# Kernel tuning notes

Hardware: AMD Instinct MI355X
Metric: run time of the kernel (lower is better)

## Reference

```python
import jax, jax.numpy as jnp
import numpy as np

L = 24        # n_layer
E = 1024      # n_emb
H = 4 * E     # ffn hidden
V = 50277     # vocab
LN_EPS = 1e-5


def _ln(x, w, b):
    m = x.mean(-1, keepdims=True)
    v = ((x - m) ** 2).mean(-1, keepdims=True)
    return (x - m) / jnp.sqrt(v + LN_EPS) * w + b


def setup_inputs() -> dict:
    key = jax.random.key(0)
    ks = jax.random.split(key, 24)
    s = 1.0 / np.sqrt(E)      # keep matvec outputs O(1) so exp-recurrence is stable
    sh = 1.0 / np.sqrt(H)
    inp = {
        "emb":      jax.random.normal(ks[0], (V, E), jnp.float32) * 0.02,
        "ln0_w":    jnp.ones((E,), jnp.float32),
        "ln0_b":    jnp.zeros((E,), jnp.float32),
        "ln1_w":    jnp.ones((L, E), jnp.float32),
        "ln1_b":    jnp.zeros((L, E), jnp.float32),
        "att_tmk":  jax.random.uniform(ks[1], (L, E), jnp.float32),
        "att_tmv":  jax.random.uniform(ks[2], (L, E), jnp.float32),
        "att_tmr":  jax.random.uniform(ks[3], (L, E), jnp.float32),
        "att_tf":   jax.random.normal(ks[4], (L, E), jnp.float32) * 0.3,
        # checkpoint stores raw time_decay; loader applies -exp(.)
        "att_td":   -jnp.exp(jax.random.normal(ks[5], (L, E), jnp.float32) * 0.3),
        "att_kw":   jax.random.normal(ks[6], (L, E, E), jnp.float32) * s,
        "att_vw":   jax.random.normal(ks[7], (L, E, E), jnp.float32) * s,
        "att_rw":   jax.random.normal(ks[8], (L, E, E), jnp.float32) * s,
        "att_ow":   jax.random.normal(ks[9], (L, E, E), jnp.float32) * s,
        "ln2_w":    jnp.ones((L, E), jnp.float32),
        "ln2_b":    jnp.zeros((L, E), jnp.float32),
        "ffn_tmk":  jax.random.uniform(ks[10], (L, E), jnp.float32),
        "ffn_tmr":  jax.random.uniform(ks[11], (L, E), jnp.float32),
        "ffn_kw":   jax.random.normal(ks[12], (L, H, E), jnp.float32) * s,
        "ffn_vw":   jax.random.normal(ks[13], (L, E, H), jnp.float32) * sh,
        "ffn_rw":   jax.random.normal(ks[14], (L, E, E), jnp.float32) * s,
        "ln_out_w": jnp.ones((E,), jnp.float32),
        "ln_out_b": jnp.zeros((E,), jnp.float32),
        "head_w":   jax.random.normal(ks[15], (V, E), jnp.float32) * s,
        "token":    123,
    }
    state = jnp.zeros((5 * L, E), jnp.float32)
    state = state.at[4::5].set(-1e30)  # pp slot, as in empty_state()
    inp["state"] = state
    return inp


def _rwkv_forward(emb, ln0_w, ln0_b, ln1_w, ln1_b, att_tmk, att_tmv, att_tmr,
                  att_tf, att_td, att_kw, att_vw, att_rw, att_ow,
                  ln2_w, ln2_b, ffn_tmk, ffn_tmr, ffn_kw, ffn_vw, ffn_rw,
                  ln_out_w, ln_out_b, head_w, state, token):
    x = emb[token]
    x = _ln(x, ln0_w, ln0_b)           # blocks.0.ln0 applied once before layer 0
    st = state.reshape(L, 5, E)        # slots: (ffn_x, att_x, aa, bb, pp)

    def step(x, inp):
        (s, l1w, l1b, tmk, tmv, tmr, tf, td, kw, vw, rw, ow,
         l2w, l2b, ftmk, ftmr, fkw, fvw, frw) = inp
        ffn_x, att_x, aa, bb, pp = s[0], s[1], s[2], s[3], s[4]
        # --- time-mix (SA) ---
        xn = _ln(x, l1w, l1b)
        xk = xn * tmk + att_x * (1 - tmk)
        xv = xn * tmv + att_x * (1 - tmv)
        xr = xn * tmr + att_x * (1 - tmr)
        r = jax.nn.sigmoid(rw @ xr)
        k = kw @ xk
        v = vw @ xv
        # numerically-stabilized WKV output
        ww = tf + k
        p = jnp.maximum(pp, ww)
        e1 = jnp.exp(pp - p)
        e2 = jnp.exp(ww - p)
        a = e1 * aa + e2 * v
        b = e1 * bb + e2
        # state update
        ww2 = pp + td
        p2 = jnp.maximum(ww2, k)
        f1 = jnp.exp(ww2 - p2)
        f2 = jnp.exp(k - p2)
        naa = f1 * aa + f2 * v
        nbb = f1 * bb + f2
        npp = p2
        sx = x + ow @ (r * a / b)
        # --- channel-mix (FF) ---
        xn2 = _ln(sx, l2w, l2b)
        fxk = xn2 * ftmk + ffn_x * (1 - ftmk)
        fxr = xn2 * ftmr + ffn_x * (1 - ftmr)
        fr = jax.nn.sigmoid(frw @ fxr)
        fk = jnp.square(jax.nn.relu(fkw @ fxk))
        out = sx + fr * (fvw @ fk)
        new_s = jnp.stack([xn2, xn, naa, nbb, npp])
        return out, new_s

    xs = (st, ln1_w, ln1_b, att_tmk, att_tmv, att_tmr, att_tf, att_td,
          att_kw, att_vw, att_rw, att_ow, ln2_w, ln2_b, ffn_tmk, ffn_tmr,
          ffn_kw, ffn_vw, ffn_rw)
    x, new_st = jax.lax.scan(step, x, xs)
    logits = head_w @ _ln(x, ln_out_w, ln_out_b)
    return logits, new_st.reshape(5 * L, E)


def reference(emb, ln0_w, ln0_b, ln1_w, ln1_b, att_tmk, att_tmv, att_tmr,
              att_tf, att_td, att_kw, att_vw, att_rw, att_ow,
              ln2_w, ln2_b, ffn_tmk, ffn_tmr, ffn_kw, ffn_vw, ffn_rw,
              ln_out_w, ln_out_b, head_w, state, token):
    return _rwkv_forward(emb, ln0_w, ln0_b, ln1_w, ln1_b, att_tmk, att_tmv,
                         att_tmr, att_tf, att_td, att_kw, att_vw, att_rw,
                         att_ow, ln2_w, ln2_b, ffn_tmk, ffn_tmr, ffn_kw,
                         ffn_vw, ffn_rw, ln_out_w, ln_out_b, head_w,
                         state, token)
```

## Files before the change

### kernel.cpp

```cpp
#include <hip/hip_runtime.h>

#define E 1024
#define H 4096
#define NLAYER 24
#define V 50277
#define NB 256
#define NT 1024
#define LN_EPS 1e-5f

typedef unsigned long long u64;

#define R1O    0
#define R2O    16384
#define POOLO  32768
#define SXO    36864
#define SSXO   37888
#define FXRO   38912
#define REDO   39936
#define PARTO  39968
#define PART2O 39984
#define SMEMF  40000

struct Params {
  const float* emb;   const float* ln0_w; const float* ln0_b;
  const float* ln1_w; const float* ln1_b;
  const float* tmk;   const float* tmv;   const float* tmr;
  const float* tf;    const float* td;
  const float* kw;    const float* vw;    const float* rw;  const float* ow;
  const float* ln2_w; const float* ln2_b;
  const float* ftmk;  const float* ftmr;
  const float* fkw;   const float* fvw;   const float* frw;
  const float* lnow;  const float* lnob;  const float* headw;
  const float* st;    const int* tok;
  float* out; float* ws;
};

__device__ __forceinline__ void stg_tag(u64* p, float v, unsigned tag) {
  u64 w = ((u64)__float_as_uint(v) << 32) | (u64)tag;
  __hip_atomic_store(p, w, __ATOMIC_RELAXED, __HIP_MEMORY_SCOPE_AGENT);
}
__device__ __forceinline__ u64 ld_tag(const u64* p) {
  return __hip_atomic_load(p, __ATOMIC_RELAXED, __HIP_MEMORY_SCOPE_AGENT);
}
__device__ __forceinline__ float poll_tag(const u64* p, unsigned tag) {
  u64 w = ld_tag(p);
  while ((unsigned)w != tag) { __builtin_amdgcn_s_sleep(1); w = ld_tag(p); }
  return __uint_as_float((unsigned)(w >> 32));
}

__device__ __forceinline__ void wait_pf() {
  asm volatile("s_waitcnt vmcnt(0)" ::: "memory");
}

__device__ __forceinline__ void gload_lds16(const float* g, float* l) {
  __builtin_amdgcn_global_load_lds(
      (const __attribute__((address_space(1))) unsigned int*)(g),
      (__attribute__((address_space(3))) unsigned int*)(l), 16, 0, 0);
}
__device__ __forceinline__ void pf_row4k(const float* row, float* dst, int lane) {
#pragma unroll
  for (int c = 0; c < 4; ++c)
    gload_lds16(row + c * 256 + lane * 4, dst + c * 256);
}

__device__ __forceinline__ float warp_sum(float v) {
#pragma unroll
  for (int off = 32; off; off >>= 1) v += __shfl_down(v, off);
  return v;
}

__device__ __forceinline__ float2 ln_stats(float v, float* red) {
  float a = v, b = v * v;
#pragma unroll
  for (int off = 32; off; off >>= 1) { a += __shfl_xor(a, off); b += __shfl_xor(b, off); }
  const int wid = threadIdx.x >> 6, lane = threadIdx.x & 63;
  if (lane == 0) { red[2 * wid] = a; red[2 * wid + 1] = b; }
  __syncthreads();
  float s1 = 0.f, s2 = 0.f;
  const float2* r2 = (const float2*)red;
#pragma unroll
  for (int j = 0; j < 16; ++j) { float2 t = r2[j]; s1 += t.x; s2 += t.y; }
  float m = s1 * (1.f / E);
  return make_float2(m, s2 * (1.f / E) - m * m);
}

__device__ __forceinline__ float dot4(float4 a, float4 b) {
  return a.x * b.x + a.y * b.y + a.z * b.z + a.w * b.w;
}

__device__ __forceinline__ float dotlds(const float* wrow, const float* vec, int lane) {
  const float4* w4 = (const float4*)wrow;
  const float4* v4 = (const float4*)vec;
  float acc = 0.f;
#pragma unroll
  for (int p = 0; p < 4; ++p)
    acc += dot4(w4[lane + p * 64], v4[lane + p * 64]);
  return warp_sum(acc);
}

__global__ __launch_bounds__(NT, 1) void rwkv_kernel(Params p) {
  const int tid = threadIdx.x, bid = blockIdx.x;
  const int lane = tid & 63, wid = tid >> 6;

  extern __shared__ float smem[];
  float* r1     = smem + R1O;
  float* r2     = smem + R2O;
  float* pool   = smem + POOLO;
  float* s_x    = smem + SXO;
  float* s_sx   = smem + SSXO;
  float* s_fxr  = smem + FXRO;
  float* s_red  = smem + REDO;
  float* s_part = smem + PARTO;
  float* s_part2= smem + PART2O;

  u64* tws = (u64*)p.ws;
  u64* tk  = tws;
  u64* tv  = tws + 2 * E;
  u64* tr  = tws + 4 * E;
  u64* tsx = tws + 6 * E;
  u64* tx  = tws + 8 * E;
  u64* tfk = tws + 10 * E;

  float* out_st = p.out + V;
  const int token = p.tok[0];

  const bool hasA = wid < 12;
  const int rA = bid * 12 + wid;
  const int matA = rA >> 10, rmA = rA & (E - 1);
  const int rloc = wid >> 2, kc = wid & 3;
  const int rowO = bid * 4 + rloc;
  float* wA = r1 + wid * 1024;
  float* wD = r2 + rloc * 4096 + kc * 1024;

  if (hasA) {
    const float* W = (matA == 0 ? p.kw : matA == 1 ? p.vw : p.rw) + (size_t)rmA * E;
    pf_row4k(W, wA, lane);
  }

  {
    float v = p.emb[(size_t)token * E + tid];
    float2 mv = ln_stats(v, s_red);
    s_x[tid] = (v - mv.x) / sqrtf(mv.y + LN_EPS) * p.ln0_w[tid] + p.ln0_b[tid];
  }

  for (int l = 0; l < NLAYER; ++l) {
    const float* stl = p.st + (size_t)5 * l * E;
    float* ostl = out_st + (size_t)5 * l * E;
    const int par = l & 1;
    const unsigned tg = (unsigned)(l + 1);

    float l1w = p.ln1_w[l * E + tid], l1b = p.ln1_b[l * E + tid];
    float ax = stl[E + tid];
    float ta = p.tmk[l * E + tid], tb = p.tmv[l * E + tid], tc = p.tmr[l * E + tid];
    float xv_;
    if (l > 0) { xv_ = poll_tag(&tx[par * E + tid], (unsigned)l); s_x[tid] = xv_; }
    else       { xv_ = s_x[tid]; }
    {
      float2 mv = ln_stats(xv_, s_red);
      float xn = (xv_ - mv.x) / sqrtf(mv.y + LN_EPS) * l1w + l1b;
      pool[tid]        = xn * ta + ax * (1.f - ta);
      pool[1024 + tid] = xn * tb + ax * (1.f - tb);
      pool[2048 + tid] = xn * tc + ax * (1.f - tc);
      if (bid == 0) ostl[E + tid] = xn;
    }
    __syncthreads();
    wait_pf();
    if (hasA) {
      float d = dotlds(wA, pool + matA * 1024, lane);
      if (lane == 0) {
        u64* dst = (matA == 0 ? tk : matA == 1 ? tv : tr) + par * E + rmA;
        stg_tag(dst, matA == 2 ? 1.f / (1.f + expf(-d)) : d, tg);
      }
    }

    {
      float aav = stl[2 * E + tid], bbv = stl[3 * E + tid], ppv = stl[4 * E + tid];
      float tfv = p.tf[l * E + tid], tdv = p.td[l * E + tid];
      float4 wow = ((const float4*)(p.ow + (size_t)l * E * E + (size_t)rowO * E + kc * 256))[lane];
      pf_row4k(p.fkw + (size_t)l * H * E + (size_t)(bid * 16 + wid) * E, wA, lane);
      const u64 *bk = tk + par * E + tid, *bv = tv + par * E + tid, *br = tr + par * E + tid;
      u64 wk = ld_tag(bk), wv = ld_tag(bv), wr = ld_tag(br);
      while ((unsigned)wk != tg) { __builtin_amdgcn_s_sleep(1); wk = ld_tag(bk); }
      while ((unsigned)wv != tg) { __builtin_amdgcn_s_sleep(1); wv = ld_tag(bv); }
      while ((unsigned)wr != tg) { __builtin_amdgcn_s_sleep(1); wr = ld_tag(br); }
      float kk = __uint_as_float((unsigned)(wk >> 32));
      float vv = __uint_as_float((unsigned)(wv >> 32));
      float rr = __uint_as_float((unsigned)(wr >> 32));
      float wwv = tfv + kk;
      float pm = fmaxf(ppv, wwv);
      float e1 = expf(ppv - pm), e2 = expf(wwv - pm);
      float a = e1 * aav + e2 * vv, b = e1 * bbv + e2;
      pool[3072 + tid] = rr * a / b;
      float ww2 = ppv + tdv;
      float p2 = fmaxf(ww2, kk);
      float f1 = expf(ww2 - p2), f2 = expf(kk - p2);
      if (bid == 0) {
        ostl[2 * E + tid] = f1 * aav + f2 * vv;
        ostl[3 * E + tid] = f1 * bbv + f2;
        ostl[4 * E + tid] = p2;
      }
      __syncthreads();
      const float4* v4 = (const float4*)(pool + 3072 + kc * 256);
      float acc = warp_sum(dot4(wow, v4[lane]));
      if (lane == 0) s_part[wid] = acc;
    }
    __syncthreads();
    if (tid < 4) {
      float dsum = s_part[tid * 4] + s_part[tid * 4 + 1] +
                   s_part[tid * 4 + 2] + s_part[tid * 4 + 3];
      stg_tag(&tsx[par * E + bid * 4 + tid], s_x[bid * 4 + tid] + dsum, tg);
    }

    {
      float l2w = p.ln2_w[l * E + tid], l2b = p.ln2_b[l * E + tid];
      float fx = stl[tid];
      float fa = p.ftmk[l * E + tid], fb = p.ftmr[l * E + tid];
      float4 wfr = ((const float4*)(p.frw + (size_t)l * E * E + (size_t)rowO * E + kc * 256))[lane];
      pf_row4k(p.fvw + (size_t)l * E * H + (size_t)rowO * H + kc * 1024, wD, lane);
      float sxv = poll_tag(&tsx[par * E + tid], tg);
      s_sx[tid] = sxv;
      float2 mv = ln_stats(sxv, s_red);
      float xn2 = (sxv - mv.x) / sqrtf(mv.y + LN_EPS) * l2w + l2b;
      pool[tid]  = xn2 * fa + fx * (1.f - fa);
      s_fxr[tid] = xn2 * fb + fx * (1.f - fb);
      if (bid == 0) ostl[tid] = xn2;
      __syncthreads();
      float d = dotlds(wA, pool, lane);
      if (lane == 0) { float t = fmaxf(d, 0.f); stg_tag(&tfk[par * H + bid * 16 + wid], t * t, tg); }
      const float4* f4 = (const float4*)(s_fxr + kc * 256);
      float fp = warp_sum(dot4(wfr, f4[lane]));
      if (lane == 0) s_part2[wid] = fp;
    }

    if (l + 1 < NLAYER && hasA) {
      const float* W = (matA == 0 ? p.kw : matA == 1 ? p.vw : p.rw) +
                       (size_t)(l + 1) * E * E + (size_t)rmA * E;
      pf_row4k(W, wA, lane);
    }
    __syncthreads();
    {
      const u64* base = tfk + par * H;
      u64 w0 = ld_tag(base + tid);
      u64 w1 = ld_tag(base + tid + 1024);
      u64 w2 = ld_tag(base + tid + 2048);
      u64 w3 = ld_tag(base + tid + 3072);
      while ((unsigned)w0 != tg) { __builtin_amdgcn_s_sleep(1); w0 = ld_tag(base + tid); }
      while ((unsigned)w1 != tg) { __builtin_amdgcn_s_sleep(1); w1 = ld_tag(base + tid + 1024); }
      while ((unsigned)w2 != tg) { __builtin_amdgcn_s_sleep(1); w2 = ld_tag(base + tid + 2048); }
      while ((unsigned)w3 != tg) { __builtin_amdgcn_s_sleep(1); w3 = ld_tag(base + tid + 3072); }
      pool[tid]        = __uint_as_float((unsigned)(w0 >> 32));
      pool[tid + 1024] = __uint_as_float((unsigned)(w1 >> 32));
      pool[tid + 2048] = __uint_as_float((unsigned)(w2 >> 32));
      pool[tid + 3072] = __uint_as_float((unsigned)(w3 >> 32));
    }
    __syncthreads();
    {
      const float4* v4 = (const float4*)(pool + kc * 1024);
      const float4* w4 = (const float4*)wD;
      float acc = 0.f;
#pragma unroll
      for (int pc = 0; pc < 4; ++pc)
        acc += dot4(w4[lane + pc * 64], v4[lane + pc * 64]);
      acc = warp_sum(acc);
      if (lane == 0) s_part[wid] = acc;
    }
    __syncthreads();
    if (tid < 4) {
      float dsum = s_part[tid * 4] + s_part[tid * 4 + 1] +
                   s_part[tid * 4 + 2] + s_part[tid * 4 + 3];
      float frs  = s_part2[tid * 4] + s_part2[tid * 4 + 1] +
                   s_part2[tid * 4 + 2] + s_part2[tid * 4 + 3];
      float fr = 1.f / (1.f + expf(-frs));
      stg_tag(&tx[((l + 1) & 1) * E + bid * 4 + tid],
              s_sx[bid * 4 + tid] + fr * dsum, tg);
    }
  }

  {
    float xv_ = poll_tag(&tx[(NLAYER & 1) * E + tid], (unsigned)NLAYER);
    float2 mv = ln_stats(xv_, s_red);
    pool[tid] = (xv_ - mv.x) / sqrtf(mv.y + LN_EPS) * p.lnow[tid] + p.lnob[tid];
  }
  __syncthreads();
  {
    const int gw = bid * 16 + wid;
    const float4* v4 = (const float4*)pool;
    float4 x0 = v4[lane], x1 = v4[lane + 64], x2 = v4[lane + 128], x3 = v4[lane + 192];
    int row = gw;
    for (; row + 12288 < V; row += 16384) {
      const float4* W0 = (const float4*)(p.headw + (size_t)row * E);
      const float4* W1 = (const float4*)(p.headw + (size_t)(row + 4096) * E);
      const float4* W2 = (const float4*)(p.headw + (size_t)(row + 8192) * E);
      const float4* W3 = (const float4*)(p.headw + (size_t)(row + 12288) * E);
      float a0 = 0.f, a1 = 0.f, a2 = 0.f, a3 = 0.f;
      a0 += dot4(W0[lane], x0) + dot4(W0[lane + 64], x1) + dot4(W0[lane + 128], x2) + dot4(W0[lane + 192], x3);
      a1 += dot4(W1[lane], x0) + dot4(W1[lane + 64], x1) + dot4(W1[lane + 128], x2) + dot4(W1[lane + 192], x3);
      a2 += dot4(W2[lane], x0) + dot4(W2[lane + 64], x1) + dot4(W2[lane + 128], x2) + dot4(W2[lane + 192], x3);
      a3 += dot4(W3[lane], x0) + dot4(W3[lane + 64], x1) + dot4(W3[lane + 128], x2) + dot4(W3[lane + 192], x3);
      a0 = warp_sum(a0); a1 = warp_sum(a1); a2 = warp_sum(a2); a3 = warp_sum(a3);
      if (lane == 0) {
        p.out[row] = a0; p.out[row + 4096] = a1;
        p.out[row + 8192] = a2; p.out[row + 12288] = a3;
      }
    }
    for (; row < V; row += 4096) {
      const float4* W0 = (const float4*)(p.headw + (size_t)row * E);
      float a0 = dot4(W0[lane], x0) + dot4(W0[lane + 64], x1) +
                 dot4(W0[lane + 128], x2) + dot4(W0[lane + 192], x3);
      a0 = warp_sum(a0);
      if (lane == 0) p.out[row] = a0;
    }
  }
}

extern "C" void kernel_launch(void* const* d_in, const int* in_sizes, int n_in,
                              void* d_out, int out_size, void* d_ws, size_t ws_size,
                              hipStream_t stream) {
  Params p;
  p.emb   = (const float*)d_in[0];
  p.ln0_w = (const float*)d_in[1];
  p.ln0_b = (const float*)d_in[2];
  p.ln1_w = (const float*)d_in[3];
  p.ln1_b = (const float*)d_in[4];
  p.tmk   = (const float*)d_in[5];
  p.tmv   = (const float*)d_in[6];
  p.tmr   = (const float*)d_in[7];
  p.tf    = (const float*)d_in[8];
  p.td    = (const float*)d_in[9];
  p.kw    = (const float*)d_in[10];
  p.vw    = (const float*)d_in[11];
  p.rw    = (const float*)d_in[12];
  p.ow    = (const float*)d_in[13];
  p.ln2_w = (const float*)d_in[14];
  p.ln2_b = (const float*)d_in[15];
  p.ftmk  = (const float*)d_in[16];
  p.ftmr  = (const float*)d_in[17];
  p.fkw   = (const float*)d_in[18];
  p.fvw   = (const float*)d_in[19];
  p.frw   = (const float*)d_in[20];
  p.lnow  = (const float*)d_in[21];
  p.lnob  = (const float*)d_in[22];
  p.headw = (const float*)d_in[23];
  if (in_sizes[24] == 1) {
    p.tok = (const int*)d_in[24];
    p.st  = (const float*)d_in[25];
  } else {
    p.st  = (const float*)d_in[24];
    p.tok = (const int*)d_in[25];
  }
  p.out   = (float*)d_out;
  p.ws    = (float*)d_ws;

  hipMemsetAsync(d_ws, 0, (10 * E + 2 * H) * sizeof(unsigned long long), stream);

  void* args[] = { &p };
  hipLaunchCooperativeKernel((const void*)rwkv_kernel, dim3(NB), dim3(NT),
                             args, SMEMF * sizeof(float), stream);
}
```

Before: 550.2 us.

## Add 512-block, 512-thread cooperative kernel variant with occupancy-checked fallback

Adds a second persistent kernel that runs 512 blocks of 512 threads, two per CU, each thread handling two embedding elements, with a smaller shared-memory footprint. The FFN value weights are now read straight from global memory into registers instead of staged in LDS. The kw/vw/rw/ow rows for the next layer are prefetched during the current layer. The host checks occupancy and falls back to the original 1024-thread kernel if two blocks per CU cannot be co-resident. The aim is more blocks to spread the per-layer matvecs and their latency; the cost is more tagged-flag polling traffic and heavier per-thread work.

```diff
diff --git a/kernel.cpp b/kernel.cpp
--- a/kernel.cpp
+++ b/kernel.cpp
@@ -4,22 +4,9 @@
 #define H 4096
 #define NLAYER 24
 #define V 50277
-#define NB 256
-#define NT 1024
 #define LN_EPS 1e-5f
 
 typedef unsigned long long u64;
-
-#define R1O    0
-#define R2O    16384
-#define POOLO  32768
-#define SXO    36864
-#define SSXO   37888
-#define FXRO   38912
-#define REDO   39936
-#define PARTO  39968
-#define PART2O 39984
-#define SMEMF  40000
 
 struct Params {
   const float* emb;   const float* ln0_w; const float* ln0_b;
@@ -47,6 +34,11 @@
   while ((unsigned)w != tag) { __builtin_amdgcn_s_sleep(1); w = ld_tag(p); }
   return __uint_as_float((unsigned)(w >> 32));
 }
+#define TAGWAIT(w, ptr, tagv) \
+  while ((unsigned)(w) != (tagv)) { __builtin_amdgcn_s_sleep(1); (w) = ld_tag(ptr); }
+__device__ __forceinline__ float tagval(u64 w) {
+  return __uint_as_float((unsigned)(w >> 32));
+}
 
 __device__ __forceinline__ void wait_pf() {
   asm volatile("s_waitcnt vmcnt(0)" ::: "memory");
@@ -69,7 +61,21 @@
   return v;
 }
 
-__device__ __forceinline__ float2 ln_stats(float v, float* red) {
+__device__ __forceinline__ float dot4(float4 a, float4 b) {
+  return a.x * b.x + a.y * b.y + a.z * b.z + a.w * b.w;
+}
+
+__device__ __forceinline__ float dotlds(const float* wrow, const float* vec, int lane) {
+  const float4* w4 = (const float4*)wrow;
+  const float4* v4 = (const float4*)vec;
+  float acc = 0.f;
+#pragma unroll
+  for (int p = 0; p < 4; ++p)
+    acc += dot4(w4[lane + p * 64], v4[lane + p * 64]);
+  return warp_sum(acc);
+}
+
+__device__ __forceinline__ float2 ln_stats_w16(float v, float* red) {
   float a = v, b = v * v;
 #pragma unroll
   for (int off = 32; off; off >>= 1) { a += __shfl_xor(a, off); b += __shfl_xor(b, off); }
@@ -84,34 +90,45 @@
   return make_float2(m, s2 * (1.f / E) - m * m);
 }
 
-__device__ __forceinline__ float dot4(float4 a, float4 b) {
-  return a.x * b.x + a.y * b.y + a.z * b.z + a.w * b.w;
-}
-
-__device__ __forceinline__ float dotlds(const float* wrow, const float* vec, int lane) {
-  const float4* w4 = (const float4*)wrow;
-  const float4* v4 = (const float4*)vec;
-  float acc = 0.f;
-#pragma unroll
-  for (int p = 0; p < 4; ++p)
-    acc += dot4(w4[lane + p * 64], v4[lane + p * 64]);
-  return warp_sum(acc);
-}
-
-__global__ __launch_bounds__(NT, 1) void rwkv_kernel(Params p) {
+__device__ __forceinline__ float2 ln_stats_w8(float a, float b, float* red) {
+#pragma unroll
+  for (int off = 32; off; off >>= 1) { a += __shfl_xor(a, off); b += __shfl_xor(b, off); }
+  const int wid = threadIdx.x >> 6, lane = threadIdx.x & 63;
+  if (lane == 0) { red[2 * wid] = a; red[2 * wid + 1] = b; }
+  __syncthreads();
+  float s1 = 0.f, s2 = 0.f;
+  const float2* r2 = (const float2*)red;
+#pragma unroll
+  for (int j = 0; j < 8; ++j) { float2 t = r2[j]; s1 += t.x; s2 += t.y; }
+  float m = s1 * (1.f / E);
+  return make_float2(m, s2 * (1.f / E) - m * m);
+}
+
+#define A_R1O    0
+#define A_R2O    16384
+#define A_POOLO  32768
+#define A_SXO    36864
+#define A_SSXO   37888
+#define A_FXRO   38912
+#define A_REDO   39936
+#define A_PARTO  39968
+#define A_PART2O 39984
+#define A_SMEMF  40000
+
+__global__ __launch_bounds__(1024, 1) void rwkv_kernel_1024(Params p) {
   const int tid = threadIdx.x, bid = blockIdx.x;
   const int lane = tid & 63, wid = tid >> 6;
 
   extern __shared__ float smem[];
-  float* r1     = smem + R1O;
-  float* r2     = smem + R2O;
-  float* pool   = smem + POOLO;
-  float* s_x    = smem + SXO;
-  float* s_sx   = smem + SSXO;
-  float* s_fxr  = smem + FXRO;
-  float* s_red  = smem + REDO;
-  float* s_part = smem + PARTO;
-  float* s_part2= smem + PART2O;
+  float* r1     = smem + A_R1O;
+  float* r2     = smem + A_R2O;
+  float* pool   = smem + A_POOLO;
+  float* s_x    = smem + A_SXO;
+  float* s_sx   = smem + A_SSXO;
+  float* s_fxr  = smem + A_FXRO;
+  float* s_red  = smem + A_REDO;
+  float* s_part = smem + A_PARTO;
+  float* s_part2= smem + A_PART2O;
 
   u64* tws = (u64*)p.ws;
   u64* tk  = tws;
@@ -139,7 +156,7 @@
 
   {
     float v = p.emb[(size_t)token * E + tid];
-    float2 mv = ln_stats(v, s_red);
+    float2 mv = ln_stats_w16(v, s_red);
     s_x[tid] = (v - mv.x) / sqrtf(mv.y + LN_EPS) * p.ln0_w[tid] + p.ln0_b[tid];
   }
 
@@ -156,7 +173,7 @@
     if (l > 0) { xv_ = poll_tag(&tx[par * E + tid], (unsigned)l); s_x[tid] = xv_; }
     else       { xv_ = s_x[tid]; }
     {
-      float2 mv = ln_stats(xv_, s_red);
+      float2 mv = ln_stats_w16(xv_, s_red);
       float xn = (xv_ - mv.x) / sqrtf(mv.y + LN_EPS) * l1w + l1b;
       pool[tid]        = xn * ta + ax * (1.f - ta);
       pool[1024 + tid] = xn * tb + ax * (1.f - tb);
@@ -180,12 +197,8 @@
       pf_row4k(p.fkw + (size_t)l * H * E + (size_t)(bid * 16 + wid) * E, wA, lane);
       const u64 *bk = tk + par * E + tid, *bv = tv + par * E + tid, *br = tr + par * E + tid;
       u64 wk = ld_tag(bk), wv = ld_tag(bv), wr = ld_tag(br);
-      while ((unsigned)wk != tg) { __builtin_amdgcn_s_sleep(1); wk = ld_tag(bk); }
-      while ((unsigned)wv != tg) { __builtin_amdgcn_s_sleep(1); wv = ld_tag(bv); }
-      while ((unsigned)wr != tg) { __builtin_amdgcn_s_sleep(1); wr = ld_tag(br); }
-      float kk = __uint_as_float((unsigned)(wk >> 32));
-      float vv = __uint_as_float((unsigned)(wv >> 32));
-      float rr = __uint_as_float((unsigned)(wr >> 32));
+      TAGWAIT(wk, bk, tg); TAGWAIT(wv, bv, tg); TAGWAIT(wr, br, tg);
+      float kk = tagval(wk), vv = tagval(wv), rr = tagval(wr);
       float wwv = tfv + kk;
       float pm = fmaxf(ppv, wwv);
       float e1 = expf(ppv - pm), e2 = expf(wwv - pm);
@@ -219,7 +232,7 @@
       pf_row4k(p.fvw + (size_t)l * E * H + (size_t)rowO * H + kc * 1024, wD, lane);
       float sxv = poll_tag(&tsx[par * E + tid], tg);
       s_sx[tid] = sxv;
-      float2 mv = ln_stats(sxv, s_red);
+      float2 mv = ln_stats_w16(sxv, s_red);
       float xn2 = (sxv - mv.x) / sqrtf(mv.y + LN_EPS) * l2w + l2b;
       pool[tid]  = xn2 * fa + fx * (1.f - fa);
       s_fxr[tid] = xn2 * fb + fx * (1.f - fb);
@@ -244,14 +257,12 @@
       u64 w1 = ld_tag(base + tid + 1024);
       u64 w2 = ld_tag(base + tid + 2048);
       u64 w3 = ld_tag(base + tid + 3072);
-      while ((unsigned)w0 != tg) { __builtin_amdgcn_s_sleep(1); w0 = ld_tag(base + tid); }
-      while ((unsigned)w1 != tg) { __builtin_amdgcn_s_sleep(1); w1 = ld_tag(base + tid + 1024); }
-      while ((unsigned)w2 != tg) { __builtin_amdgcn_s_sleep(1); w2 = ld_tag(base + tid + 2048); }
-      while ((unsigned)w3 != tg) { __builtin_amdgcn_s_sleep(1); w3 = ld_tag(base + tid + 3072); }
-      pool[tid]        = __uint_as_float((unsigned)(w0 >> 32));
-      pool[tid + 1024] = __uint_as_float((unsigned)(w1 >> 32));
-      pool[tid + 2048] = __uint_as_float((unsigned)(w2 >> 32));
-      pool[tid + 3072] = __uint_as_float((unsigned)(w3 >> 32));
+      TAGWAIT(w0, base + tid, tg);        TAGWAIT(w1, base + tid + 1024, tg);
+      TAGWAIT(w2, base + tid + 2048, tg); TAGWAIT(w3, base + tid + 3072, tg);
+      pool[tid]        = tagval(w0);
+      pool[tid + 1024] = tagval(w1);
+      pool[tid + 2048] = tagval(w2);
+      pool[tid + 3072] = tagval(w3);
     }
     __syncthreads();
     {
@@ -278,12 +289,291 @@
 
   {
     float xv_ = poll_tag(&tx[(NLAYER & 1) * E + tid], (unsigned)NLAYER);
-    float2 mv = ln_stats(xv_, s_red);
+    float2 mv = ln_stats_w16(xv_, s_red);
     pool[tid] = (xv_ - mv.x) / sqrtf(mv.y + LN_EPS) * p.lnow[tid] + p.lnob[tid];
   }
   __syncthreads();
   {
     const int gw = bid * 16 + wid;
+    const float4* v4 = (const float4*)pool;
+    float4 x0 = v4[lane], x1 = v4[lane + 64], x2 = v4[lane + 128], x3 = v4[lane + 192];
+    int row = gw;
+    for (; row + 12288 < V; row += 16384) {
+      const float4* W0 = (const float4*)(p.headw + (size_t)row * E);
+      const float4* W1 = (const float4*)(p.headw + (size_t)(row + 4096) * E);
+      const float4* W2 = (const float4*)(p.headw + (size_t)(row + 8192) * E);
+      const float4* W3 = (const float4*)(p.headw + (size_t)(row + 12288) * E);
+      float a0 = 0.f, a1 = 0.f, a2 = 0.f, a3 = 0.f;
+      a0 += dot4(W0[lane], x0) + dot4(W0[lane + 64], x1) + dot4(W0[lane + 128], x2) + dot4(W0[lane + 192], x3);
+      a1 += dot4(W1[lane], x0) + dot4(W1[lane + 64], x1) + dot4(W1[lane + 128], x2) + dot4(W1[lane + 192], x3);
+      a2 += dot4(W2[lane], x0) + dot4(W2[lane + 64], x1) + dot4(W2[lane + 128], x2) + dot4(W2[lane + 192], x3);
+      a3 += dot4(W3[lane], x0) + dot4(W3[lane + 64], x1) + dot4(W3[lane + 128], x2) + dot4(W3[lane + 192], x3);
+      a0 = warp_sum(a0); a1 = warp_sum(a1); a2 = warp_sum(a2); a3 = warp_sum(a3);
+      if (lane == 0) {
+        p.out[row] = a0; p.out[row + 4096] = a1;
+        p.out[row + 8192] = a2; p.out[row + 12288] = a3;
+      }
+    }
+    for (; row < V; row += 4096) {
+      const float4* W0 = (const float4*)(p.headw + (size_t)row * E);
+      float a0 = dot4(W0[lane], x0) + dot4(W0[lane + 64], x1) +
+                 dot4(W0[lane + 128], x2) + dot4(W0[lane + 192], x3);
+      a0 = warp_sum(a0);
+      if (lane == 0) p.out[row] = a0;
+    }
+  }
+}
+
+#define B_R1O    0
+#define B_POOLO  8192
+#define B_SXO    12288
+#define B_SSXO   13312
+#define B_REDO   14336
+#define B_PARTO  14368
+#define B_PART2O 14384
+#define B_SMEMF  14400
+
+__global__ __launch_bounds__(512, 4) void rwkv_kernel_512(Params p) {
+  const int tid = threadIdx.x, bid = blockIdx.x;
+  const int lane = tid & 63, wid = tid >> 6;
+  const int e0 = tid, e1 = tid + 512;
+
+  extern __shared__ float smem[];
+  float* r1     = smem + B_R1O;
+  float* pool   = smem + B_POOLO;
+  float* s_x    = smem + B_SXO;
+  float* s_sx   = smem + B_SSXO;
+  float* s_red  = smem + B_REDO;
+  float* s_part = smem + B_PARTO;
+  float* s_part2= smem + B_PART2O;
+
+  u64* tws = (u64*)p.ws;
+  u64* tk  = tws;
+  u64* tv  = tws + 2 * E;
+  u64* tr  = tws + 4 * E;
+  u64* tsx = tws + 6 * E;
+  u64* tx  = tws + 8 * E;
+  u64* tfk = tws + 10 * E;
+
+  float* out_st = p.out + V;
+  const int token = p.tok[0];
+
+  const bool hasA = wid < 6;
+  const int rA = bid * 6 + wid;
+  const int matA = rA >> 10, rmA = rA & (E - 1);
+  const int rloc = wid >> 2, kc = wid & 3;
+  const int rowO = bid * 2 + rloc;
+  float* wA = r1 + wid * 1024;
+
+  if (hasA) {
+    const float* W = (matA == 0 ? p.kw : matA == 1 ? p.vw : p.rw) + (size_t)rmA * E;
+    pf_row4k(W, wA, lane);
+  } else {
+    pf_row4k(p.ow + (size_t)(bid * 2 + wid - 6) * E, wA, lane);
+  }
+
+  {
+    float v0 = p.emb[(size_t)token * E + e0];
+    float v1 = p.emb[(size_t)token * E + e1];
+    float2 mv = ln_stats_w8(v0 + v1, v0 * v0 + v1 * v1, s_red);
+    float is = 1.f / sqrtf(mv.y + LN_EPS);
+    s_x[e0] = (v0 - mv.x) * is * p.ln0_w[e0] + p.ln0_b[e0];
+    s_x[e1] = (v1 - mv.x) * is * p.ln0_w[e1] + p.ln0_b[e1];
+  }
+
+  for (int l = 0; l < NLAYER; ++l) {
+    const float* stl = p.st + (size_t)5 * l * E;
+    float* ostl = out_st + (size_t)5 * l * E;
+    const int par = l & 1;
+    const unsigned tg = (unsigned)(l + 1);
+
+    float l1w0 = p.ln1_w[l * E + e0], l1b0 = p.ln1_b[l * E + e0];
+    float l1w1 = p.ln1_w[l * E + e1], l1b1 = p.ln1_b[l * E + e1];
+    float ax0 = stl[E + e0], ax1 = stl[E + e1];
+    float ta0 = p.tmk[l * E + e0], tb0 = p.tmv[l * E + e0], tc0 = p.tmr[l * E + e0];
+    float ta1 = p.tmk[l * E + e1], tb1 = p.tmv[l * E + e1], tc1 = p.tmr[l * E + e1];
+    float xv0, xv1;
+    if (l > 0) {
+      const u64 *a0 = &tx[par * E + e0], *a1 = &tx[par * E + e1];
+      u64 w0 = ld_tag(a0), w1 = ld_tag(a1);
+      TAGWAIT(w0, a0, (unsigned)l); TAGWAIT(w1, a1, (unsigned)l);
+      xv0 = tagval(w0); xv1 = tagval(w1);
+      s_x[e0] = xv0; s_x[e1] = xv1;
+    } else { xv0 = s_x[e0]; xv1 = s_x[e1]; }
+    {
+      float2 mv = ln_stats_w8(xv0 + xv1, xv0 * xv0 + xv1 * xv1, s_red);
+      float is = 1.f / sqrtf(mv.y + LN_EPS);
+      float xn0 = (xv0 - mv.x) * is * l1w0 + l1b0;
+      float xn1 = (xv1 - mv.x) * is * l1w1 + l1b1;
+      pool[e0]        = xn0 * ta0 + ax0 * (1.f - ta0);
+      pool[e1]        = xn1 * ta1 + ax1 * (1.f - ta1);
+      pool[1024 + e0] = xn0 * tb0 + ax0 * (1.f - tb0);
+      pool[1024 + e1] = xn1 * tb1 + ax1 * (1.f - tb1);
+      pool[2048 + e0] = xn0 * tc0 + ax0 * (1.f - tc0);
+      pool[2048 + e1] = xn1 * tc1 + ax1 * (1.f - tc1);
+      if (bid == 0) { ostl[E + e0] = xn0; ostl[E + e1] = xn1; }
+    }
+    __syncthreads();
+    wait_pf();
+    if (hasA) {
+      float d = dotlds(wA, pool + matA * 1024, lane);
+      if (lane == 0) {
+        u64* dst = (matA == 0 ? tk : matA == 1 ? tv : tr) + par * E + rmA;
+        stg_tag(dst, matA == 2 ? 1.f / (1.f + expf(-d)) : d, tg);
+      }
+    }
+
+    {
+      float aav0 = stl[2 * E + e0], bbv0 = stl[3 * E + e0], ppv0 = stl[4 * E + e0];
+      float aav1 = stl[2 * E + e1], bbv1 = stl[3 * E + e1], ppv1 = stl[4 * E + e1];
+      float tfv0 = p.tf[l * E + e0], tdv0 = p.td[l * E + e0];
+      float tfv1 = p.tf[l * E + e1], tdv1 = p.td[l * E + e1];
+      float4 wow = ((const float4*)(p.ow + (size_t)l * E * E + (size_t)rowO * E + kc * 256))[lane];
+      if (wid < 6)
+        pf_row4k(p.fkw + (size_t)l * H * E + (size_t)(bid * 8 + wid) * E, wA, lane);
+      const u64 *pk0 = &tk[par * E + e0], *pv0 = &tv[par * E + e0], *pr0 = &tr[par * E + e0];
+      const u64 *pk1 = &tk[par * E + e1], *pv1 = &tv[par * E + e1], *pr1 = &tr[par * E + e1];
+      u64 qk0 = ld_tag(pk0), qv0 = ld_tag(pv0), qr0 = ld_tag(pr0);
+      u64 qk1 = ld_tag(pk1), qv1 = ld_tag(pv1), qr1 = ld_tag(pr1);
+      TAGWAIT(qk0, pk0, tg); TAGWAIT(qv0, pv0, tg); TAGWAIT(qr0, pr0, tg);
+      TAGWAIT(qk1, pk1, tg); TAGWAIT(qv1, pv1, tg); TAGWAIT(qr1, pr1, tg);
+      float kk0 = tagval(qk0), vv0 = tagval(qv0), rr0 = tagval(qr0);
+      float kk1 = tagval(qk1), vv1 = tagval(qv1), rr1 = tagval(qr1);
+      {
+        float wwv = tfv0 + kk0;
+        float pm = fmaxf(ppv0, wwv);
+        float ee1 = expf(ppv0 - pm), ee2 = expf(wwv - pm);
+        float a = ee1 * aav0 + ee2 * vv0, b = ee1 * bbv0 + ee2;
+        pool[3072 + e0] = rr0 * a / b;
+        float ww2 = ppv0 + tdv0;
+        float p2 = fmaxf(ww2, kk0);
+        float f1 = expf(ww2 - p2), f2 = expf(kk0 - p2);
+        if (bid == 0) {
+          ostl[2 * E + e0] = f1 * aav0 + f2 * vv0;
+          ostl[3 * E + e0] = f1 * bbv0 + f2;
+          ostl[4 * E + e0] = p2;
+        }
+      }
+      {
+        float wwv = tfv1 + kk1;
+        float pm = fmaxf(ppv1, wwv);
+        float ee1 = expf(ppv1 - pm), ee2 = expf(wwv - pm);
+        float a = ee1 * aav1 + ee2 * vv1, b = ee1 * bbv1 + ee2;
+        pool[3072 + e1] = rr1 * a / b;
+        float ww2 = ppv1 + tdv1;
+        float p2 = fmaxf(ww2, kk1);
+        float f1 = expf(ww2 - p2), f2 = expf(kk1 - p2);
+        if (bid == 0) {
+          ostl[2 * E + e1] = f1 * aav1 + f2 * vv1;
+          ostl[3 * E + e1] = f1 * bbv1 + f2;
+          ostl[4 * E + e1] = p2;
+        }
+      }
+      __syncthreads();
+      const float4* v4 = (const float4*)(pool + 3072 + kc * 256);
+      float acc = warp_sum(dot4(wow, v4[lane]));
+      if (lane == 0) s_part[wid] = acc;
+    }
+    __syncthreads();
+    if (wid >= 6)
+      pf_row4k(p.fkw + (size_t)l * H * E + (size_t)(bid * 8 + wid) * E, wA, lane);
+    if (tid < 2) {
+      float dsum = s_part[tid * 4] + s_part[tid * 4 + 1] +
+                   s_part[tid * 4 + 2] + s_part[tid * 4 + 3];
+      stg_tag(&tsx[par * E + bid * 2 + tid], s_x[bid * 2 + tid] + dsum, tg);
+    }
+
+    {
+      float l2w0 = p.ln2_w[l * E + e0], l2b0 = p.ln2_b[l * E + e0];
+      float l2w1 = p.ln2_w[l * E + e1], l2b1 = p.ln2_b[l * E + e1];
+      float fx0 = stl[e0], fx1 = stl[e1];
+      float fa0 = p.ftmk[l * E + e0], fb0 = p.ftmr[l * E + e0];
+      float fa1 = p.ftmk[l * E + e1], fb1 = p.ftmr[l * E + e1];
+      float4 wfr = ((const float4*)(p.frw + (size_t)l * E * E + (size_t)rowO * E + kc * 256))[lane];
+      const u64 *s0 = &tsx[par * E + e0], *s1 = &tsx[par * E + e1];
+      u64 w0 = ld_tag(s0), w1 = ld_tag(s1);
+      TAGWAIT(w0, s0, tg); TAGWAIT(w1, s1, tg);
+      float sxv0 = tagval(w0), sxv1 = tagval(w1);
+      s_sx[e0] = sxv0; s_sx[e1] = sxv1;
+      float2 mv = ln_stats_w8(sxv0 + sxv1, sxv0 * sxv0 + sxv1 * sxv1, s_red);
+      float is = 1.f / sqrtf(mv.y + LN_EPS);
+      float xn20 = (sxv0 - mv.x) * is * l2w0 + l2b0;
+      float xn21 = (sxv1 - mv.x) * is * l2w1 + l2b1;
+      pool[e0]        = xn20 * fa0 + fx0 * (1.f - fa0);
+      pool[e1]        = xn21 * fa1 + fx1 * (1.f - fa1);
+      pool[1024 + e0] = xn20 * fb0 + fx0 * (1.f - fb0);
+      pool[1024 + e1] = xn21 * fb1 + fx1 * (1.f - fb1);
+      if (bid == 0) { ostl[e0] = xn20; ostl[e1] = xn21; }
+      __syncthreads();
+      float d = dotlds(wA, pool, lane);
+      if (lane == 0) { float t = fmaxf(d, 0.f); stg_tag(&tfk[par * H + bid * 8 + wid], t * t, tg); }
+      const float4* f4 = (const float4*)(pool + 1024 + kc * 256);
+      float fp = warp_sum(dot4(wfr, f4[lane]));
+      if (lane == 0) s_part2[wid] = fp;
+    }
+
+    if (l + 1 < NLAYER) {
+      if (hasA) {
+        const float* W = (matA == 0 ? p.kw : matA == 1 ? p.vw : p.rw) +
+                         (size_t)(l + 1) * E * E + (size_t)rmA * E;
+        pf_row4k(W, wA, lane);
+      } else {
+        pf_row4k(p.ow + (size_t)(l + 1) * E * E + (size_t)(bid * 2 + wid - 6) * E, wA, lane);
+      }
+    }
+    __syncthreads();
+    {
+      const float4* Wf = (const float4*)(p.fvw + (size_t)l * E * H + (size_t)rowO * H + kc * 1024);
+      float4 f0 = Wf[lane], f1 = Wf[lane + 64], f2 = Wf[lane + 128], f3 = Wf[lane + 192];
+      const u64* base = tfk + par * H;
+      u64 q0 = ld_tag(base + tid);
+      u64 q1 = ld_tag(base + tid + 512);
+      u64 q2 = ld_tag(base + tid + 1024);
+      u64 q3 = ld_tag(base + tid + 1536);
+      u64 q4 = ld_tag(base + tid + 2048);
+      u64 q5 = ld_tag(base + tid + 2560);
+      u64 q6 = ld_tag(base + tid + 3072);
+      u64 q7 = ld_tag(base + tid + 3584);
+      TAGWAIT(q0, base + tid, tg);        TAGWAIT(q1, base + tid + 512, tg);
+      TAGWAIT(q2, base + tid + 1024, tg); TAGWAIT(q3, base + tid + 1536, tg);
+      TAGWAIT(q4, base + tid + 2048, tg); TAGWAIT(q5, base + tid + 2560, tg);
+      TAGWAIT(q6, base + tid + 3072, tg); TAGWAIT(q7, base + tid + 3584, tg);
+      pool[tid]        = tagval(q0); pool[tid + 512]  = tagval(q1);
+      pool[tid + 1024] = tagval(q2); pool[tid + 1536] = tagval(q3);
+      pool[tid + 2048] = tagval(q4); pool[tid + 2560] = tagval(q5);
+      pool[tid + 3072] = tagval(q6); pool[tid + 3584] = tagval(q7);
+      __syncthreads();
+      const float4* v4 = (const float4*)(pool + kc * 1024);
+      float acc = dot4(f0, v4[lane]) + dot4(f1, v4[lane + 64]) +
+                  dot4(f2, v4[lane + 128]) + dot4(f3, v4[lane + 192]);
+      acc = warp_sum(acc);
+      if (lane == 0) s_part[wid] = acc;
+    }
+    __syncthreads();
+    if (tid < 2) {
+      float dsum = s_part[tid * 4] + s_part[tid * 4 + 1] +
+                   s_part[tid * 4 + 2] + s_part[tid * 4 + 3];
+      float frs  = s_part2[tid * 4] + s_part2[tid * 4 + 1] +
+                   s_part2[tid * 4 + 2] + s_part2[tid * 4 + 3];
+      float fr = 1.f / (1.f + expf(-frs));
+      stg_tag(&tx[((l + 1) & 1) * E + bid * 2 + tid],
+              s_sx[bid * 2 + tid] + fr * dsum, tg);
+    }
+  }
+
+  {
+    const u64 *a0 = &tx[(NLAYER & 1) * E + e0], *a1 = &tx[(NLAYER & 1) * E + e1];
+    u64 w0 = ld_tag(a0), w1 = ld_tag(a1);
+    TAGWAIT(w0, a0, (unsigned)NLAYER); TAGWAIT(w1, a1, (unsigned)NLAYER);
+    float xv0 = tagval(w0), xv1 = tagval(w1);
+    float2 mv = ln_stats_w8(xv0 + xv1, xv0 * xv0 + xv1 * xv1, s_red);
+    float is = 1.f / sqrtf(mv.y + LN_EPS);
+    pool[e0] = (xv0 - mv.x) * is * p.lnow[e0] + p.lnob[e0];
+    pool[e1] = (xv1 - mv.x) * is * p.lnow[e1] + p.lnob[e1];
+  }
+  __syncthreads();
+  {
+    const int gw = bid * 8 + wid;
     const float4* v4 = (const float4*)pool;
     float4 x0 = v4[lane], x1 = v4[lane + 64], x2 = v4[lane + 128], x3 = v4[lane + 192];
     int row = gw;
@@ -353,7 +643,16 @@
 
   hipMemsetAsync(d_ws, 0, (10 * E + 2 * H) * sizeof(unsigned long long), stream);
 
+  int maxb = 0;
+  hipError_t qerr = hipOccupancyMaxActiveBlocksPerMultiprocessor(
+      &maxb, (const void*)rwkv_kernel_512, 512, (size_t)B_SMEMF * sizeof(float));
   void* args[] = { &p };
-  hipLaunchCooperativeKernel((const void*)rwkv_kernel, dim3(NB), dim3(NT),
-                             args, SMEMF * sizeof(float), stream);
-}
+  if (qerr == hipSuccess && maxb >= 2) {
+    hipError_t lerr = hipLaunchCooperativeKernel((const void*)rwkv_kernel_512,
+                                                 dim3(512), dim3(512), args,
+                                                 B_SMEMF * sizeof(float), stream);
+    if (lerr == hipSuccess) return;
+  }
+  hipLaunchCooperativeKernel((const void*)rwkv_kernel_1024, dim3(256), dim3(1024),
+                             args, A_SMEMF * sizeof(float), stream);
+}
```

Result: no change. 547.1 us (-0.5%).
